# Optimization experiments

Hardware: AMD Instinct MI355X
Metric: run time of the kernel (lower is better)

The kernel has to match this reference:

```python
import jax, jax.numpy as jnp
import numpy as np

B, S, D, H = 4, 2048, 1024, 16
HD = D // H

def setup_inputs() -> dict:
    key = jax.random.key(0)
    ks = jax.random.split(key, 11)
    scale = 1.0 / np.sqrt(D)
    return {
        "query": jax.random.normal(ks[0], (B, S, D), jnp.float32),
        "key_": jax.random.normal(ks[1], (B, S, D), jnp.float32),
        "value": jax.random.normal(ks[2], (B, S, D), jnp.float32),
        "wq": jax.random.normal(ks[3], (D, D), jnp.float32) * scale,
        "bq": jnp.zeros((D,), jnp.float32),
        "wk": jax.random.normal(ks[4], (D, D), jnp.float32) * scale,
        "bk": jnp.zeros((D,), jnp.float32),
        "wv": jax.random.normal(ks[5], (D, D), jnp.float32) * scale,
        "bv": jnp.zeros((D,), jnp.float32),
        "wo": jax.random.normal(ks[6], (D, D), jnp.float32) * scale,
        "bo": jnp.zeros((D,), jnp.float32),
    }

def _split_heads(x):
    b, s, _ = x.shape
    return x.reshape(b, s, H, HD).transpose(0, 2, 1, 3)  # [B,H,S,HD]

def reference(query, key_, value, wq, bq, wk, bk, wv, bv, wo, bo):
    q = _split_heads(query @ wq + bq)
    k = _split_heads(key_ @ wk + bk)
    v = _split_heads(value @ wv + bv)
    scores = jnp.einsum('bhqd,bhkd->bhqk', q, k) / jnp.sqrt(jnp.float32(HD))
    attn = jax.nn.softmax(scores, axis=-1)
    ctx = jnp.einsum('bhqk,bhkd->bhqd', attn, v)
    ctx = ctx.transpose(0, 2, 1, 3).reshape(B, S, D)
    return ctx @ wo + bo
```

## Files before the change

kernel.cpp:

```cpp
#include <hip/hip_runtime.h>

typedef _Float16 f16;
typedef _Float16 f16x8 __attribute__((ext_vector_type(8)));
typedef _Float16 f16x4 __attribute__((ext_vector_type(4)));
typedef float    f32x4 __attribute__((ext_vector_type(4)));
typedef float    f32x16 __attribute__((ext_vector_type(16)));

#define MROWS 8192
#define KDIM  1024
#define SEQ   2048
#define HDIM  64
#define QKV_LD 3072

#if __has_builtin(__builtin_amdgcn_exp2f)
#define EXP2(x) __builtin_amdgcn_exp2f(x)
#else
#define EXP2(x) exp2f(x)
#endif

__device__ __forceinline__ int swz5(int row) { return (row ^ (row >> 3)) & 7; }

__global__ __launch_bounds__(256) void cast3_k(const float* __restrict__ a,
                                               const float* __restrict__ b,
                                               const float* __restrict__ c,
                                               f16* __restrict__ out) {
  int i = blockIdx.x * 256 + threadIdx.x;
  const float* src = (blockIdx.y == 0) ? a : (blockIdx.y == 1) ? b : c;
  float4 v = ((const float4*)src)[i];
  f16x4 o = { (f16)v.x, (f16)v.y, (f16)v.z, (f16)v.w };
  *(f16x4*)&out[(size_t)blockIdx.y * 8388608 + (size_t)i * 4] = o;
}

__global__ __launch_bounds__(256) void transpose_cast_k(const float* __restrict__ w,
                                                        f16* __restrict__ wt) {
  __shared__ float t[32][33];
  int tx = threadIdx.x, ty = threadIdx.y;
  int bx = blockIdx.x * 32, by = blockIdx.y * 32;
  #pragma unroll
  for (int i = ty; i < 32; i += 8) t[i][tx] = w[(size_t)(by + i) * KDIM + bx + tx];
  __syncthreads();
  #pragma unroll
  for (int i = ty; i < 32; i += 8) wt[(size_t)(bx + i) * KDIM + by + tx] = (f16)t[tx][i];
}

__global__ __launch_bounds__(256) void concat3_k(const float* __restrict__ a,
                                                 const float* __restrict__ b,
                                                 const float* __restrict__ c,
                                                 float* __restrict__ o) {
  int i = blockIdx.x * 256 + threadIdx.x;
  float v;
  if (i < 1024) v = a[i]; else if (i < 2048) v = b[i - 1024]; else v = c[i - 2048];
  o[i] = v;
}

template<bool OUT_F16>
__global__ __launch_bounds__(256) void gemm_k(const f16* __restrict__ A0, size_t aStride,
                                              const f16* __restrict__ Bt,
                                              const float* __restrict__ bias,
                                              void* __restrict__ Cout, int ldc) {
  __shared__ f16 sA[128 * 64];
  __shared__ f16 sB[128 * 64];
  const int tid  = threadIdx.x;
  const int lane = tid & 63;
  const int r    = lane & 15;
  const int q    = lane >> 4;
  const int wave = tid >> 6;
  const int m0 = blockIdx.x * 128;
  const int ng = blockIdx.z * 1024 + blockIdx.y * 128;
  const int wm = (wave >> 1) * 64;
  const int wn = (wave & 1) * 64;
  const f16* A = A0 + (size_t)blockIdx.z * aStride;

  f32x4 acc[4][4];
  #pragma unroll
  for (int i = 0; i < 4; ++i)
    #pragma unroll
    for (int j = 0; j < 4; ++j) acc[i][j] = (f32x4){0.f, 0.f, 0.f, 0.f};

  for (int kt = 0; kt < KDIM; kt += 64) {
    #pragma unroll
    for (int issue = 0; issue < 4; ++issue) {
      int g   = issue * 256 + tid;
      int row = g >> 3;
      int csw = (g & 7) ^ (row & 7);
      const f16* gA = A  + (size_t)(m0 + row) * KDIM + kt + csw * 8;
      const f16* gB = Bt + (size_t)(ng + row) * KDIM + kt + csw * 8;
      int lb = __builtin_amdgcn_readfirstlane((issue * 256 + (tid & ~63)) * 16);
      __builtin_amdgcn_global_load_lds((const __attribute__((address_space(1))) void*)gA,
                                       (__attribute__((address_space(3))) void*)((char*)sA + lb),
                                       16, 0, 0);
      __builtin_amdgcn_global_load_lds((const __attribute__((address_space(1))) void*)gB,
                                       (__attribute__((address_space(3))) void*)((char*)sB + lb),
                                       16, 0, 0);
    }
    __syncthreads();
    #pragma unroll
    for (int kk = 0; kk < 64; kk += 32) {
      f16x8 af[4], bf[4];
      #pragma unroll
      for (int mi = 0; mi < 4; ++mi) {
        int row = wm + mi * 16 + r;
        int cs  = ((kk >> 3) + q) ^ (row & 7);
        af[mi] = *(const f16x8*)&sA[row * 64 + cs * 8];
      }
      #pragma unroll
      for (int ni = 0; ni < 4; ++ni) {
        int row = wn + ni * 16 + r;
        int cs  = ((kk >> 3) + q) ^ (row & 7);
        bf[ni] = *(const f16x8*)&sB[row * 64 + cs * 8];
      }
      #pragma unroll
      for (int mi = 0; mi < 4; ++mi)
        #pragma unroll
        for (int ni = 0; ni < 4; ++ni)
          acc[mi][ni] = __builtin_amdgcn_mfma_f32_16x16x32_f16(af[mi], bf[ni], acc[mi][ni], 0, 0, 0);
    }
    __syncthreads();
  }
  #pragma unroll
  for (int ni = 0; ni < 4; ++ni) {
    int col = ng + wn + ni * 16 + r;
    float bv = bias[col];
    #pragma unroll
    for (int mi = 0; mi < 4; ++mi) {
      int rowb = m0 + wm + mi * 16 + q * 4;
      #pragma unroll
      for (int reg = 0; reg < 4; ++reg) {
        float v = acc[mi][ni][reg] + bv;
        if constexpr (OUT_F16) ((f16*)Cout)[(size_t)(rowb + reg) * ldc + col] = (f16)v;
        else                   ((float*)Cout)[(size_t)(rowb + reg) * ldc + col] = v;
      }
    }
  }
}

__global__ __launch_bounds__(256) void vtrans_k(const f16* __restrict__ qkv,
                                                f16* __restrict__ vt) {
  __shared__ f16 t[64 * 64];
  const int tid = threadIdx.x;
  const int st = blockIdx.x, h = blockIdx.y, b = blockIdx.z;
  const f16* src = qkv + (size_t)(b * SEQ + st * 64) * QKV_LD + 2048 + h * HDIM;
  #pragma unroll
  for (int issue = 0; issue < 2; ++issue) {
    int g = issue * 256 + tid;
    int srow = g >> 3, c = g & 7;
    f16x8 v = *(const f16x8*)(src + (size_t)srow * QKV_LD + c * 8);
    *(f16x8*)&t[srow * 64 + (c ^ (srow & 7)) * 8] = v;
  }
  __syncthreads();
  f16* dst = vt + (size_t)(b * 16 + h) * HDIM * SEQ + st * 64;
  #pragma unroll
  for (int issue = 0; issue < 2; ++issue) {
    int g = issue * 256 + tid;
    int d = g >> 3, c8 = g & 7;
    f16x8 o;
    #pragma unroll
    for (int j = 0; j < 8; ++j) {
      int s = c8 * 8 + j;
      o[j] = t[s * 64 + ((d >> 3) ^ (s & 7)) * 8 + (d & 7)];
    }
    *(f16x8*)(dst + (size_t)d * SEQ + c8 * 8) = o;
  }
}

__global__ __launch_bounds__(256) void attn_k(const f16* __restrict__ qkv,
                                              const f16* __restrict__ vt,
                                              f16* __restrict__ ctx) {
  __shared__ f16 smem[16384];
  const int tid  = threadIdx.x;
  const int lane = tid & 63;
  const int wave = tid >> 6;
  const int n    = lane & 31;
  const int q32  = lane >> 5;
  const int flat = blockIdx.x + (blockIdx.y << 4) + (blockIdx.z << 8);
  const int qt = flat >> 6;
  const int h  = flat & 15;
  const int b  = (flat >> 4) & 3;

  const f16* Qb  = qkv + (size_t)b * SEQ * QKV_LD + h * HDIM;
  const f16* Vtb = vt + (size_t)(b * 16 + h) * HDIM * SEQ;
  const int qrow = qt * 128 + wave * 32 + n;

  f16x8 qf[4];
  {
    const f16* qp = Qb + (size_t)qrow * QKV_LD + q32 * 8;
    const f16 sc = (f16)(0.125f * 1.44269504f);
    #pragma unroll
    for (int cc = 0; cc < 4; ++cc) qf[cc] = *(const f16x8*)(qp + cc * 16) * sc;
  }

  const int r0 = tid >> 3, c0 = tid & 7;
  const f16* gK0 = Qb + 1024 + (size_t)r0 * QKV_LD + (c0 ^ swz5(r0)) * 8;
  const f16* gK1 = Qb + 1024 + (size_t)(r0 + 32) * QKV_LD + (c0 ^ swz5(r0 + 32)) * 8;
  const f16* gV0 = Vtb + (size_t)r0 * SEQ + (c0 ^ swz5(r0)) * 8;
  const f16* gV1 = Vtb + (size_t)(r0 + 32) * SEQ + (c0 ^ swz5(r0 + 32)) * 8;
  const int lb = __builtin_amdgcn_readfirstlane((tid & ~63) * 16);

  auto stage = [&](int bufbyte) {
    char* base = (char*)smem + bufbyte + lb;
    __builtin_amdgcn_global_load_lds((const __attribute__((address_space(1))) void*)gK0,
                                     (__attribute__((address_space(3))) void*)(base), 16, 0, 0);
    __builtin_amdgcn_global_load_lds((const __attribute__((address_space(1))) void*)gK1,
                                     (__attribute__((address_space(3))) void*)(base + 4096), 16, 0, 0);
    __builtin_amdgcn_global_load_lds((const __attribute__((address_space(1))) void*)gV0,
                                     (__attribute__((address_space(3))) void*)(base + 8192), 16, 0, 0);
    __builtin_amdgcn_global_load_lds((const __attribute__((address_space(1))) void*)gV1,
                                     (__attribute__((address_space(3))) void*)(base + 12288), 16, 0, 0);
    gK0 += 64 * QKV_LD; gK1 += 64 * QKV_LD; gV0 += 64; gV1 += 64;
  };

  f32x16 ot[2];
  #pragma unroll
  for (int db = 0; db < 2; ++db)
    #pragma unroll
    for (int i = 0; i < 16; ++i) ot[db][i] = 0.f;
  float ls = 0.f;

  auto compute = [&](int bufe) {
    const f16* sK = smem + bufe;
    const f16* sV = smem + bufe + 4096;
    f16x4 p[2][4];
    #pragma unroll
    for (int kc = 0; kc < 2; ++kc) {
      f32x16 st;
      #pragma unroll
      for (int i = 0; i < 16; ++i) st[i] = -2.8853901817f;
      __builtin_amdgcn_s_setprio(1);
      #pragma unroll
      for (int cc = 0; cc < 4; ++cc) {
        int row = kc * 32 + n;
        f16x8 kf = *(const f16x8*)&sK[row * 64 + (((cc * 2 + q32) ^ swz5(row)) * 8)];
        st = __builtin_amdgcn_mfma_f32_32x32x16_f16(kf, qf[cc], st, 0, 0, 0);
      }
      __builtin_amdgcn_s_setprio(0);
      #pragma unroll
      for (int g = 0; g < 4; ++g) {
        float e0 = EXP2(st[4 * g + 0]);
        float e1 = EXP2(st[4 * g + 1]);
        float e2 = EXP2(st[4 * g + 2]);
        float e3 = EXP2(st[4 * g + 3]);
        ls += (e0 + e1) + (e2 + e3);
        p[kc][g] = (f16x4){ (f16)e0, (f16)e1, (f16)e2, (f16)e3 };
      }
    }
    __builtin_amdgcn_s_setprio(1);
    #pragma unroll
    for (int db = 0; db < 2; ++db) {
      int row = db * 32 + n;
      int fr = swz5(row);
      const f16* vrow = &sV[row * 64];
      #pragma unroll
      for (int cc = 0; cc < 4; ++cc) {
        int hg = (2 * cc) ^ fr;
        f16x4 vlo = *(const f16x4*)&vrow[hg * 8 + q32 * 4];
        f16x4 vhi = *(const f16x4*)&vrow[(hg ^ 1) * 8 + q32 * 4];
        f16x8 vf = __builtin_shufflevector(vlo, vhi, 0, 1, 2, 3, 4, 5, 6, 7);
        f16x8 pf = __builtin_shufflevector(p[cc >> 1][2 * (cc & 1)],
                                           p[cc >> 1][2 * (cc & 1) + 1],
                                           0, 1, 2, 3, 4, 5, 6, 7);
        ot[db] = __builtin_amdgcn_mfma_f32_32x32x16_f16(vf, pf, ot[db], 0, 0, 0);
      }
    }
    __builtin_amdgcn_s_setprio(0);
  };

  stage(0);
  #pragma unroll 1
  for (int it = 0; it < 32; it += 2) {
    __syncthreads();
    stage(16384);
    compute(0);
    __syncthreads();
    if (it + 2 < 32) stage(0);
    compute(8192);
  }

  ls += __shfl_xor(ls, 32);
  float inv = 1.0f / ls;

  f16* sO = smem;
  int nl = wave * 32 + n;
  int fo = swz5(nl);
  #pragma unroll
  for (int db = 0; db < 2; ++db)
    #pragma unroll
    for (int g = 0; g < 4; ++g) {
      f16x4 o = { (f16)(ot[db][4 * g + 0] * inv), (f16)(ot[db][4 * g + 1] * inv),
                  (f16)(ot[db][4 * g + 2] * inv), (f16)(ot[db][4 * g + 3] * inv) };
      *(f16x4*)&sO[nl * 64 + (((db * 4 + g) ^ fo) * 8) + q32 * 4] = o;
    }
  __syncthreads();
  #pragma unroll
  for (int issue = 0; issue < 4; ++issue) {
    int g = issue * 256 + tid;
    int rr = g >> 3, sg = g & 7;
    f16x8 v = *(const f16x8*)&sO[rr * 64 + ((sg ^ swz5(rr)) * 8)];
    *(f16x8*)&ctx[(size_t)(b * SEQ + qt * 128 + rr) * KDIM + h * HDIM + sg * 8] = v;
  }
}

extern "C" void kernel_launch(void* const* d_in, const int* in_sizes, int n_in,
                              void* d_out, int out_size, void* d_ws, size_t ws_size,
                              hipStream_t stream) {
  (void)in_sizes; (void)n_in; (void)out_size; (void)ws_size;
  const float* query = (const float*)d_in[0];
  const float* key_  = (const float*)d_in[1];
  const float* value = (const float*)d_in[2];
  const float* wq = (const float*)d_in[3];
  const float* bq = (const float*)d_in[4];
  const float* wk = (const float*)d_in[5];
  const float* bk = (const float*)d_in[6];
  const float* wv = (const float*)d_in[7];
  const float* bv = (const float*)d_in[8];
  const float* wo = (const float*)d_in[9];
  const float* bo = (const float*)d_in[10];
  float* out = (float*)d_out;

  char* ws = (char*)d_ws;
  f16*   X16  = (f16*)(ws);
  f16*   qkvT = (f16*)(ws + 50331648);
  f16*   woT  = (f16*)(ws + 56623104);
  float* b3   = (float*)(ws + 58720256);
  f16*   QKV  = (f16*)(ws + 58736640);
  f16*   ctx  = (f16*)(ws);
  f16*   Vt   = (f16*)(ws + 16777216);

  cast3_k<<<dim3(8192, 3), 256, 0, stream>>>(query, key_, value, X16);
  transpose_cast_k<<<dim3(32, 32), dim3(32, 8), 0, stream>>>(wq, qkvT);
  transpose_cast_k<<<dim3(32, 32), dim3(32, 8), 0, stream>>>(wk, qkvT + 1048576);
  transpose_cast_k<<<dim3(32, 32), dim3(32, 8), 0, stream>>>(wv, qkvT + 2097152);
  transpose_cast_k<<<dim3(32, 32), dim3(32, 8), 0, stream>>>(wo, woT);
  concat3_k<<<12, 256, 0, stream>>>(bq, bk, bv, b3);

  gemm_k<true><<<dim3(64, 8, 3), 256, 0, stream>>>(X16, (size_t)8388608, qkvT, b3, (void*)QKV, QKV_LD);
  vtrans_k<<<dim3(32, 16, 4), 256, 0, stream>>>(QKV, Vt);
  attn_k<<<dim3(16, 16, 4), 256, 0, stream>>>(QKV, Vt, ctx);
  gemm_k<false><<<dim3(64, 8, 1), 256, 0, stream>>>(ctx, (size_t)0, woT, bo, (void*)out, 1024);
}
```

Measured before the change: 362.8 us.

## Add 256x256-tile pipelined QKV GEMM with 512 threads and quadrant scheduling

Replaces the 128x128-tile QKV projection GEMM with a new kernel. It uses 256x256 output tiles, 8 waves per block and double-buffered LDS of 128KB. Global-to-LDS loads for the next K-steps are interleaved with MFMA work on four quadrants, using barriers, s_setprio and manual vmcnt waits. Blocks are remapped so that neighbouring blocks share A/B tiles. The goal is more data reuse per LDS byte and hiding load latency. The cost is a large LDS footprint that limits occupancy to one block per CU, and a fragile hand-tuned schedule.

```diff
diff --git a/kernel.cpp b/kernel.cpp
--- a/kernel.cpp
+++ b/kernel.cpp
@@ -17,6 +17,9 @@
 #else
 #define EXP2(x) exp2f(x)
 #endif
+
+#define AS1 __attribute__((address_space(1)))
+#define AS3 __attribute__((address_space(3)))
 
 __device__ __forceinline__ int swz5(int row) { return (row ^ (row >> 3)) & 7; }
 
@@ -86,12 +89,10 @@
       const f16* gA = A  + (size_t)(m0 + row) * KDIM + kt + csw * 8;
       const f16* gB = Bt + (size_t)(ng + row) * KDIM + kt + csw * 8;
       int lb = __builtin_amdgcn_readfirstlane((issue * 256 + (tid & ~63)) * 16);
-      __builtin_amdgcn_global_load_lds((const __attribute__((address_space(1))) void*)gA,
-                                       (__attribute__((address_space(3))) void*)((char*)sA + lb),
-                                       16, 0, 0);
-      __builtin_amdgcn_global_load_lds((const __attribute__((address_space(1))) void*)gB,
-                                       (__attribute__((address_space(3))) void*)((char*)sB + lb),
-                                       16, 0, 0);
+      __builtin_amdgcn_global_load_lds((const AS1 void*)gA,
+                                       (AS3 void*)((char*)sA + lb), 16, 0, 0);
+      __builtin_amdgcn_global_load_lds((const AS1 void*)gB,
+                                       (AS3 void*)((char*)sB + lb), 16, 0, 0);
     }
     __syncthreads();
     #pragma unroll
@@ -130,6 +131,150 @@
         if constexpr (OUT_F16) ((f16*)Cout)[(size_t)(rowb + reg) * ldc + col] = (f16)v;
         else                   ((float*)Cout)[(size_t)(rowb + reg) * ldc + col] = v;
       }
+    }
+  }
+}
+
+__global__ __launch_bounds__(512, 2) void gemm256_k(const f16* __restrict__ A0,
+                                                    const f16* __restrict__ Bt,
+                                                    const float* __restrict__ bias,
+                                                    f16* __restrict__ Cout) {
+  __shared__ f16 smem[65536];
+  const int tid  = threadIdx.x;
+  const int lane = tid & 63;
+  const int r    = lane & 15;
+  const int q    = lane >> 4;
+  const int wave = tid >> 6;
+  const int wm   = wave >> 2;
+  const int wn   = wave & 3;
+
+  const int id  = blockIdx.x;
+  const int swz = (id & 7) * 48 + (id >> 3);
+  const int bx  = swz & 31;
+  const int by  = swz >> 5;
+  const int m0  = bx * 256;
+  const int n0  = by * 256;
+  const f16* A  = A0 + (size_t)(by >> 2) * 8388608;
+
+  const int srow0 = tid >> 3;
+  const int srow1 = (512 + tid) >> 3;
+  const int sg0 = (tid & 7) ^ (srow0 & 7);
+  const int sg1 = (tid & 7) ^ (srow1 & 7);
+  const f16* gA0 = A  + (size_t)(m0 + srow0) * KDIM + sg0 * 8;
+  const f16* gA1 = A  + (size_t)(m0 + srow1) * KDIM + sg1 * 8;
+  const f16* gB0 = Bt + (size_t)(n0 + srow0) * KDIM + sg0 * 8;
+  const f16* gB1 = Bt + (size_t)(n0 + srow1) * KDIM + sg1 * 8;
+  const int lb0 = __builtin_amdgcn_readfirstlane((tid & ~63) * 16);
+  const int lb1 = __builtin_amdgcn_readfirstlane((512 + (tid & ~63)) * 16);
+
+  auto issueA = [&](int s, int hi) {
+    char* base = (char*)smem + (s & 1) * 65536 + hi * 16384;
+    const f16* s0 = gA0 + (size_t)hi * (128 * KDIM) + s * 64;
+    const f16* s1 = gA1 + (size_t)hi * (128 * KDIM) + s * 64;
+    __builtin_amdgcn_global_load_lds((const AS1 void*)s0, (AS3 void*)(base + lb0), 16, 0, 0);
+    __builtin_amdgcn_global_load_lds((const AS1 void*)s1, (AS3 void*)(base + lb1), 16, 0, 0);
+  };
+  auto issueB = [&](int s, int hi) {
+    char* base = (char*)smem + (s & 1) * 65536 + 32768 + hi * 16384;
+    const f16* s0 = gB0 + (size_t)hi * (128 * KDIM) + s * 64;
+    const f16* s1 = gB1 + (size_t)hi * (128 * KDIM) + s * 64;
+    __builtin_amdgcn_global_load_lds((const AS1 void*)s0, (AS3 void*)(base + lb0), 16, 0, 0);
+    __builtin_amdgcn_global_load_lds((const AS1 void*)s1, (AS3 void*)(base + lb1), 16, 0, 0);
+  };
+
+  auto readA = [&](int s, int qa, f16x8 (&af)[4][2]) {
+    const f16* rg = smem + (s & 1) * 32768 + qa * 8192;
+    #pragma unroll
+    for (int mi = 0; mi < 4; ++mi) {
+      int rl = wm * 64 + mi * 16 + r;
+      #pragma unroll
+      for (int kk2 = 0; kk2 < 2; ++kk2) {
+        int g = kk2 * 4 + q;
+        af[mi][kk2] = *(const f16x8*)&rg[rl * 64 + ((g ^ (rl & 7)) * 8)];
+      }
+    }
+  };
+  auto readB = [&](int s, int qb, f16x8 (&bf)[2][2]) {
+    const f16* rg = smem + (s & 1) * 32768 + 16384 + qb * 8192;
+    #pragma unroll
+    for (int ni = 0; ni < 2; ++ni) {
+      int rl = wn * 32 + ni * 16 + r;
+      #pragma unroll
+      for (int kk2 = 0; kk2 < 2; ++kk2) {
+        int g = kk2 * 4 + q;
+        bf[ni][kk2] = *(const f16x8*)&rg[rl * 64 + ((g ^ (rl & 7)) * 8)];
+      }
+    }
+  };
+
+  f32x4 acc[8][4];
+  #pragma unroll
+  for (int i = 0; i < 8; ++i)
+    #pragma unroll
+    for (int j = 0; j < 4; ++j) acc[i][j] = (f32x4){0.f, 0.f, 0.f, 0.f};
+
+  auto mmaQ = [&](f16x8 (&af)[4][2], f16x8 (&bf)[2][2], int qa, int qb) {
+    __builtin_amdgcn_s_setprio(1);
+    #pragma unroll
+    for (int kk2 = 0; kk2 < 2; ++kk2)
+      #pragma unroll
+      for (int mi = 0; mi < 4; ++mi)
+        #pragma unroll
+        for (int ni = 0; ni < 2; ++ni)
+          acc[qa * 4 + mi][qb * 2 + ni] =
+            __builtin_amdgcn_mfma_f32_16x16x32_f16(af[mi][kk2], bf[ni][kk2],
+                                                   acc[qa * 4 + mi][qb * 2 + ni], 0, 0, 0);
+    __builtin_amdgcn_s_setprio(0);
+  };
+
+  auto bar = [] {
+    __builtin_amdgcn_sched_barrier(0);
+    __builtin_amdgcn_s_barrier();
+    __builtin_amdgcn_sched_barrier(0);
+  };
+
+  issueA(0, 0); issueB(0, 0); issueB(0, 1); issueA(0, 1);
+  issueB(1, 0); issueA(1, 0); issueB(1, 1);
+  asm volatile("s_waitcnt vmcnt(6)");
+  bar();
+
+  f16x8 alo[4][2], ahi[4][2], blo[2][2], bhi[2][2];
+  #pragma unroll 1
+  for (int s = 0; s < 16; ++s) {
+    readA(s, 0, alo);
+    readB(s, 0, blo);
+    if (s + 1 < 16) issueA(s + 1, 1);
+    bar();
+    mmaQ(alo, blo, 0, 0);
+    bar();
+    readB(s, 1, bhi);
+    if (s + 2 < 16) issueB(s + 2, 0);
+    bar();
+    mmaQ(alo, bhi, 0, 1);
+    bar();
+    readA(s, 1, ahi);
+    if (s + 2 < 16) issueA(s + 2, 0);
+    bar();
+    mmaQ(ahi, bhi, 1, 1);
+    bar();
+    if (s + 2 < 16) issueB(s + 2, 1);
+    if (s < 14)       { asm volatile("s_waitcnt vmcnt(6)"); }
+    else if (s == 14) { asm volatile("s_waitcnt vmcnt(0)"); }
+    bar();
+    mmaQ(ahi, blo, 1, 0);
+    bar();
+  }
+
+  #pragma unroll
+  for (int mi8 = 0; mi8 < 8; ++mi8) {
+    int rowb = m0 + (mi8 >> 2) * 128 + wm * 64 + (mi8 & 3) * 16 + q * 4;
+    #pragma unroll
+    for (int ni4 = 0; ni4 < 4; ++ni4) {
+      int col = n0 + (ni4 >> 1) * 128 + wn * 32 + (ni4 & 1) * 16 + r;
+      float bv = bias[col];
+      #pragma unroll
+      for (int reg = 0; reg < 4; ++reg)
+        Cout[(size_t)(rowb + reg) * QKV_LD + col] = (f16)(acc[mi8][ni4][reg] + bv);
     }
   }
 }
@@ -198,14 +343,10 @@
 
   auto stage = [&](int bufbyte) {
     char* base = (char*)smem + bufbyte + lb;
-    __builtin_amdgcn_global_load_lds((const __attribute__((address_space(1))) void*)gK0,
-                                     (__attribute__((address_space(3))) void*)(base), 16, 0, 0);
-    __builtin_amdgcn_global_load_lds((const __attribute__((address_space(1))) void*)gK1,
-                                     (__attribute__((address_space(3))) void*)(base + 4096), 16, 0, 0);
-    __builtin_amdgcn_global_load_lds((const __attribute__((address_space(1))) void*)gV0,
-                                     (__attribute__((address_space(3))) void*)(base + 8192), 16, 0, 0);
-    __builtin_amdgcn_global_load_lds((const __attribute__((address_space(1))) void*)gV1,
-                                     (__attribute__((address_space(3))) void*)(base + 12288), 16, 0, 0);
+    __builtin_amdgcn_global_load_lds((const AS1 void*)gK0, (AS3 void*)(base), 16, 0, 0);
+    __builtin_amdgcn_global_load_lds((const AS1 void*)gK1, (AS3 void*)(base + 4096), 16, 0, 0);
+    __builtin_amdgcn_global_load_lds((const AS1 void*)gV0, (AS3 void*)(base + 8192), 16, 0, 0);
+    __builtin_amdgcn_global_load_lds((const AS1 void*)gV1, (AS3 void*)(base + 12288), 16, 0, 0);
     gK0 += 64 * QKV_LD; gK1 += 64 * QKV_LD; gV0 += 64; gV1 += 64;
   };
 
@@ -332,7 +473,7 @@
   transpose_cast_k<<<dim3(32, 32), dim3(32, 8), 0, stream>>>(wo, woT);
   concat3_k<<<12, 256, 0, stream>>>(bq, bk, bv, b3);
 
-  gemm_k<true><<<dim3(64, 8, 3), 256, 0, stream>>>(X16, (size_t)8388608, qkvT, b3, (void*)QKV, QKV_LD);
+  gemm256_k<<<dim3(384), 512, 0, stream>>>(X16, qkvT, b3, QKV);
   vtrans_k<<<dim3(32, 16, 4), 256, 0, stream>>>(QKV, Vt);
   attn_k<<<dim3(16, 16, 4), 256, 0, stream>>>(QKV, Vt, ctx);
   gemm_k<false><<<dim3(64, 8, 1), 256, 0, stream>>>(ctx, (size_t)0, woT, bo, (void*)out, 1024);
```

New measurement: 363.1 us. About the same (+0.1%).
